# Performance work log

Measured on AMD Instinct MI355X. Metric: run time of the kernel, lower is better.

The kernel has to match this reference:

```python
import jax, jax.numpy as jnp
import numpy as np

N_NODES = 100000


def setup_inputs() -> dict:
    key = jax.random.key(0)
    ks = jax.random.split(key, 8)
    IN, HID, OUT = 128, 128, 64
    E = 1600000
    x = jax.random.normal(ks[0], (N_NODES, IN), dtype=jnp.float32)
    edge_index = jax.random.randint(ks[1], (2, E), 0, N_NODES, dtype=jnp.int64)
    # PyG SAGEConv params: lin_l (applied to aggregated neighbors, with bias),
    # lin_r (root weight, no bias).
    def lin(k, fi, fo):
        return jax.random.normal(k, (fi, fo), dtype=jnp.float32) / np.sqrt(fi)
    Wl0 = lin(ks[2], IN, HID)
    bl0 = jnp.zeros((HID,), dtype=jnp.float32)
    Wr0 = lin(ks[3], IN, HID)
    Wl1 = lin(ks[4], HID, OUT)
    bl1 = jnp.zeros((OUT,), dtype=jnp.float32)
    Wr1 = lin(ks[5], HID, OUT)
    return {"x": x, "edge_index": edge_index,
            "Wl0": Wl0, "bl0": bl0, "Wr0": Wr0,
            "Wl1": Wl1, "bl1": bl1, "Wr1": Wr1}


def _sage_conv(h, src, dst, Wl, bl, Wr):
    # mean aggregation of source features onto target nodes
    summed = jax.ops.segment_sum(h[src], dst, num_segments=N_NODES)  # [N, d]
    cnt = jax.ops.segment_sum(jnp.ones((src.shape[0], 1), h.dtype), dst,
                              num_segments=N_NODES)                  # [N, 1]
    agg = summed / jnp.maximum(cnt, 1.0)
    return agg @ Wl + bl + h @ Wr


def reference(x, edge_index, Wl0, bl0, Wr0, Wl1, bl1, Wr1):
    src, dst = edge_index[0], edge_index[1]
    h = jax.nn.relu(_sage_conv(x, src, dst, Wl0, bl0, Wr0))
    # dropout is identity in eval mode (training=False)
    return _sage_conv(h, src, dst, Wl1, bl1, Wr1)
```

## Files before the change

### kernel.cpp

```cpp
#include <hip/hip_runtime.h>


typedef short short8 __attribute__((ext_vector_type(8)));
typedef float f32x4 __attribute__((ext_vector_type(4)));
typedef float f32x2 __attribute__((ext_vector_type(2)));

#define NBUCK 782
#define BCAP  3072
#define EPB   8192

static __device__ __forceinline__ unsigned short f2bf(float f) {
    union { float f; unsigned u; } c; c.f = f;
    unsigned u = c.u + 0x7fffu + ((c.u >> 16) & 1u);
    return (unsigned short)(u >> 16);
}
static __device__ __forceinline__ float bf2f(unsigned short b) {
    union { unsigned u; float f; } c; c.u = ((unsigned)b) << 16;
    return c.f;
}
static __device__ __forceinline__ float bf2f_s(short b) {
    return bf2f((unsigned short)b);
}

static __device__ __forceinline__ unsigned char f2fp8(float x) {
    union { float f; unsigned u; } c; c.f = x;
    unsigned s = (c.u >> 24) & 0x80u;
    float a = __builtin_fabsf(x);
    if (a < 0.015625f) {
        int m = (int)rintf(a * 512.0f);
        return (unsigned char)(s | (unsigned)m);
    }
    unsigned u = c.u + 0x7ffffu + ((c.u >> 20) & 1u);
    int e = (int)((u >> 23) & 0xff) - 120;
    unsigned m = (u >> 20) & 7u;
    if (e > 15) { e = 15; m = 6; }
    return (unsigned char)(s | (unsigned)(e << 3) | m);
}

static __device__ __forceinline__ void acc_fp8x4(unsigned w, float* a) {
#if __has_builtin(__builtin_amdgcn_cvt_pk_f32_fp8)
    f32x2 lo = __builtin_amdgcn_cvt_pk_f32_fp8((int)w, false);
    f32x2 hi = __builtin_amdgcn_cvt_pk_f32_fp8((int)w, true);
    a[0] += lo[0]; a[1] += lo[1]; a[2] += hi[0]; a[3] += hi[1];
#else
    #pragma unroll
    for (int j = 0; j < 4; ++j) {
        unsigned b = (w >> (8 * j)) & 0xffu;
        union { unsigned u; float f; } c;
        c.u = ((b & 0x80u) << 24) | ((b & 0x7fu) << 20);
        a[j] += c.f * 0x1p120f;
    }
#endif
}

__global__ __launch_bounds__(256) void k_pack(const float* __restrict__ WA,
                                              const float* __restrict__ WB,
                                              int CA, int NC,
                                              unsigned short* __restrict__ Wp) {
    int tid = blockIdx.x * 256 + threadIdx.x;
    if (tid >= NC * 16) return;
    int lane = tid & 63, kk = (tid >> 6) & 3, tg = tid >> 8;
    int l15 = lane & 15, quad = lane >> 4;
    int c = tg * 16 + l15;
    const float* W = (c < CA) ? WA : WB;
    int cc = (c < CA) ? c : c - CA;
    short8 v;
    #pragma unroll
    for (int j = 0; j < 8; ++j) {
        int k = kk * 32 + quad * 8 + j;
        v[j] = (short)f2bf(W[(size_t)k * CA + cc]);
    }
    *(short8*)(Wp + (size_t)tid * 8) = v;
}

__global__ __launch_bounds__(256) void k_gemm0_bucket(
        const float* __restrict__ X, const unsigned short* __restrict__ Wp,
        unsigned char* __restrict__ P0, unsigned short* __restrict__ Q0, int Nrows,
        const int* __restrict__ src, const int* __restrict__ dst,
        int* __restrict__ cursor, int* __restrict__ bregion,
        int E, int gemmBlocks) {
    const int t = threadIdx.x;
    if ((int)blockIdx.x < gemmBlocks) {
        const int wave = t >> 6, lane = t & 63;
        const int quad = lane >> 4, l15 = lane & 15;
        const int row0 = blockIdx.x * 32;
        const int c0w = wave * 64;
        f32x4 acc[2][4];
        #pragma unroll
        for (int mt = 0; mt < 2; ++mt)
            #pragma unroll
            for (int tt = 0; tt < 4; ++tt) acc[mt][tt] = (f32x4){0.f, 0.f, 0.f, 0.f};
        #pragma unroll
        for (int kk = 0; kk < 4; ++kk) {
            const int k0 = kk * 32 + quad * 8;
            short8 a[2];
            #pragma unroll
            for (int mt = 0; mt < 2; ++mt) {
                int row = row0 + mt * 16 + l15;
                if (row > Nrows - 1) row = Nrows - 1;
                const float* xp = X + (size_t)row * 128 + k0;
                float4 f0 = *(const float4*)xp;
                float4 f1 = *(const float4*)(xp + 4);
                short8 v;
                v[0] = (short)f2bf(f0.x); v[1] = (short)f2bf(f0.y);
                v[2] = (short)f2bf(f0.z); v[3] = (short)f2bf(f0.w);
                v[4] = (short)f2bf(f1.x); v[5] = (short)f2bf(f1.y);
                v[6] = (short)f2bf(f1.z); v[7] = (short)f2bf(f1.w);
                a[mt] = v;
            }
            short8 b[4];
            #pragma unroll
            for (int tt = 0; tt < 4; ++tt) {
                int tg = (c0w >> 4) + tt;
                b[tt] = *(const short8*)(Wp + ((size_t)(tg * 4 + kk) * 64 + lane) * 8);
            }
            #pragma unroll
            for (int mt = 0; mt < 2; ++mt)
                #pragma unroll
                for (int tt = 0; tt < 4; ++tt)
                    acc[mt][tt] = __builtin_amdgcn_mfma_f32_16x16x32_bf16(
                        a[mt], b[tt], acc[mt][tt], 0, 0, 0);
        }
        #pragma unroll
        for (int mt = 0; mt < 2; ++mt)
            #pragma unroll
            for (int r = 0; r < 4; ++r) {
                int row = row0 + mt * 16 + quad * 4 + r;
                if (row < Nrows) {
                    if (c0w < 128) {
                        #pragma unroll
                        for (int tt = 0; tt < 4; ++tt)
                            P0[(size_t)row * 128 + c0w + tt * 16 + l15] =
                                f2fp8(acc[mt][tt][r]);
                    } else {
                        #pragma unroll
                        for (int tt = 0; tt < 4; ++tt)
                            Q0[(size_t)row * 128 + (c0w - 128) + tt * 16 + l15] =
                                f2bf(acc[mt][tt][r]);
                    }
                }
            }
        return;
    }
    __shared__ int hist[NBUCK];
    __shared__ int basel[NBUCK];
    int bid = blockIdx.x - gemmBlocks;
    for (int i = t; i < NBUCK; i += 256) hist[i] = 0;
    __syncthreads();
    int e0 = bid * EPB + t * 32;
    int d[32];
    if (e0 + 32 <= E) {
        #pragma unroll
        for (int q = 0; q < 8; ++q) {
            int4 v = *(const int4*)(dst + e0 + q * 4);
            d[q * 4 + 0] = v.x; d[q * 4 + 1] = v.y;
            d[q * 4 + 2] = v.z; d[q * 4 + 3] = v.w;
        }
    } else {
        #pragma unroll
        for (int j = 0; j < 32; ++j) d[j] = (e0 + j < E) ? dst[e0 + j] : -1;
    }
    #pragma unroll
    for (int j = 0; j < 32; ++j)
        if (d[j] >= 0) atomicAdd(&hist[d[j] >> 7], 1);
    __syncthreads();
    for (int i = t; i < NBUCK; i += 256) {
        int c = hist[i];
        basel[i] = (c > 0) ? atomicAdd(&cursor[i], c) : 0;
    }
    __syncthreads();
    for (int i = t; i < NBUCK; i += 256) hist[i] = 0;
    __syncthreads();
    int s[32];
    if (e0 + 32 <= E) {
        #pragma unroll
        for (int q = 0; q < 8; ++q) {
            int4 v = *(const int4*)(src + e0 + q * 4);
            s[q * 4 + 0] = v.x; s[q * 4 + 1] = v.y;
            s[q * 4 + 2] = v.z; s[q * 4 + 3] = v.w;
        }
    } else {
        #pragma unroll
        for (int j = 0; j < 32; ++j) s[j] = (e0 + j < E) ? src[e0 + j] : 0;
    }
    #pragma unroll
    for (int j = 0; j < 32; ++j) {
        if (d[j] < 0) continue;
        int b = d[j] >> 7;
        int r = atomicAdd(&hist[b], 1);
        bregion[(size_t)b * BCAP + basel[b] + r] = s[j] | ((d[j] & 127) << 20);
    }
}

__global__ __launch_bounds__(256) void k_csr(const int* __restrict__ cursor,
                                             const int* __restrict__ bregion,
                                             int* __restrict__ rowptr,
                                             int* __restrict__ csr, int Nn) {
    __shared__ int words[BCAP];
    __shared__ int hist[128], sc[128], rank[128];
    __shared__ int red[256];
    int b = blockIdx.x, t = threadIdx.x;
    int part = 0;
    for (int i = t; i < b; i += 256) part += cursor[i];
    red[t] = part;
    if (t < 128) { hist[t] = 0; rank[t] = 0; }
    __syncthreads();
    #pragma unroll
    for (int off = 128; off > 0; off >>= 1) {
        if (t < off) red[t] += red[t + off];
        __syncthreads();
    }
    int gbase = red[0];
    int cnt = cursor[b];
    for (int i = t; i < cnt; i += 256) {
        int w = bregion[(size_t)b * BCAP + i];
        words[i] = w;
        atomicAdd(&hist[w >> 20], 1);
    }
    __syncthreads();
    if (t < 128) sc[t] = hist[t];
    __syncthreads();
    #pragma unroll
    for (int off = 1; off < 128; off <<= 1) {
        int x = 0;
        if (t < 128 && t >= off) x = sc[t - off];
        __syncthreads();
        if (t < 128) sc[t] += x;
        __syncthreads();
    }
    if (t < 128) sc[t] -= hist[t];
    __syncthreads();
    if (t < 128) {
        int node = b * 128 + t;
        if (node <= Nn) rowptr[node] = gbase + sc[t];
    }
    for (int i = t; i < cnt; i += 256) {
        int w = words[i];
        int d7 = w >> 20;
        int r = atomicAdd(&rank[d7], 1);
        csr[gbase + sc[d7] + r] = w & 0xFFFFF;
    }
}

__global__ __launch_bounds__(256) void k_gemm1(const unsigned short* __restrict__ Xv,
                                               const unsigned short* __restrict__ Wp,
                                               unsigned char* __restrict__ P1,
                                               unsigned short* __restrict__ Q1,
                                               int Nrows) {
    const int t = threadIdx.x;
    const int wave = t >> 6, lane = t & 63;
    const int quad = lane >> 4, l15 = lane & 15;
    const int row0 = blockIdx.x * 32;
    const int c0w = wave * 32;
    f32x4 acc[2][2];
    #pragma unroll
    for (int mt = 0; mt < 2; ++mt)
        #pragma unroll
        for (int tt = 0; tt < 2; ++tt) acc[mt][tt] = (f32x4){0.f, 0.f, 0.f, 0.f};
    #pragma unroll
    for (int kk = 0; kk < 4; ++kk) {
        const int k0 = kk * 32 + quad * 8;
        short8 a[2];
        #pragma unroll
        for (int mt = 0; mt < 2; ++mt) {
            int row = row0 + mt * 16 + l15;
            if (row > Nrows - 1) row = Nrows - 1;
            a[mt] = *(const short8*)(Xv + (size_t)row * 128 + k0);
        }
        short8 b[2];
        #pragma unroll
        for (int tt = 0; tt < 2; ++tt) {
            int tg = (c0w >> 4) + tt;
            b[tt] = *(const short8*)(Wp + ((size_t)(tg * 4 + kk) * 64 + lane) * 8);
        }
        #pragma unroll
        for (int mt = 0; mt < 2; ++mt)
            #pragma unroll
            for (int tt = 0; tt < 2; ++tt)
                acc[mt][tt] = __builtin_amdgcn_mfma_f32_16x16x32_bf16(
                    a[mt], b[tt], acc[mt][tt], 0, 0, 0);
    }
    #pragma unroll
    for (int mt = 0; mt < 2; ++mt)
        #pragma unroll
        for (int r = 0; r < 4; ++r) {
            int row = row0 + mt * 16 + quad * 4 + r;
            if (row < Nrows) {
                if (c0w < 64) {
                    #pragma unroll
                    for (int tt = 0; tt < 2; ++tt)
                        P1[(size_t)row * 64 + c0w + tt * 16 + l15] =
                            f2fp8(acc[mt][tt][r]);
                } else {
                    #pragma unroll
                    for (int tt = 0; tt < 2; ++tt)
                        Q1[(size_t)row * 64 + (c0w - 64) + tt * 16 + l15] =
                            f2bf(acc[mt][tt][r]);
                }
            }
        }
}

__global__ __launch_bounds__(256) void k_agg0(const unsigned char* __restrict__ P0,
                                              const unsigned short* __restrict__ Q0,
                                              const int* __restrict__ rowptr,
                                              const int* __restrict__ csr,
                                              const float* __restrict__ bl0,
                                              unsigned short* __restrict__ h, int Nn) {
    int wave = threadIdx.x >> 6, lane = threadIdx.x & 63;
    int n = blockIdx.x * 4 + wave;
    if (n >= Nn) return;
    int g = lane >> 3, l7 = lane & 7;
    int st = rowptr[n], dg = rowptr[n + 1] - st;
    float acc[16] = {};
    int e = 0;
    for (; e + 16 <= dg; e += 16) {
        int s0 = csr[st + e + g];
        int s1 = csr[st + e + 8 + g];
        uint4 w0 = *(const uint4*)(P0 + (size_t)s0 * 128 + l7 * 16);
        uint4 w1 = *(const uint4*)(P0 + (size_t)s1 * 128 + l7 * 16);
        acc_fp8x4(w0.x, acc + 0);  acc_fp8x4(w0.y, acc + 4);
        acc_fp8x4(w0.z, acc + 8);  acc_fp8x4(w0.w, acc + 12);
        acc_fp8x4(w1.x, acc + 0);  acc_fp8x4(w1.y, acc + 4);
        acc_fp8x4(w1.z, acc + 8);  acc_fp8x4(w1.w, acc + 12);
    }
    for (; e + 8 <= dg; e += 8) {
        int s0 = csr[st + e + g];
        uint4 w0 = *(const uint4*)(P0 + (size_t)s0 * 128 + l7 * 16);
        acc_fp8x4(w0.x, acc + 0);  acc_fp8x4(w0.y, acc + 4);
        acc_fp8x4(w0.z, acc + 8);  acc_fp8x4(w0.w, acc + 12);
    }
    if (e + g < dg) {
        int s0 = csr[st + e + g];
        uint4 w0 = *(const uint4*)(P0 + (size_t)s0 * 128 + l7 * 16);
        acc_fp8x4(w0.x, acc + 0);  acc_fp8x4(w0.y, acc + 4);
        acc_fp8x4(w0.z, acc + 8);  acc_fp8x4(w0.w, acc + 12);
    }
    #pragma unroll
    for (int j = 0; j < 16; ++j) {
        acc[j] += __shfl_xor(acc[j], 8);
        acc[j] += __shfl_xor(acc[j], 16);
        acc[j] += __shfl_xor(acc[j], 32);
    }
    if (lane < 8) {
        float inv = 1.f / fmaxf((float)dg, 1.f);
        short8 q0 = *(const short8*)(Q0 + (size_t)n * 128 + l7 * 16);
        short8 q1 = *(const short8*)(Q0 + (size_t)n * 128 + l7 * 16 + 8);
        float bb[16];
        *(float4*)(bb + 0)  = *(const float4*)(bl0 + l7 * 16);
        *(float4*)(bb + 4)  = *(const float4*)(bl0 + l7 * 16 + 4);
        *(float4*)(bb + 8)  = *(const float4*)(bl0 + l7 * 16 + 8);
        *(float4*)(bb + 12) = *(const float4*)(bl0 + l7 * 16 + 12);
        short8 o0, o1;
        #pragma unroll
        for (int j = 0; j < 8; ++j) {
            float v = fmaxf(acc[j] * inv + bb[j] + bf2f_s(q0[j]), 0.f);
            o0[j] = (short)f2bf(v);
        }
        #pragma unroll
        for (int j = 0; j < 8; ++j) {
            float v = fmaxf(acc[8 + j] * inv + bb[8 + j] + bf2f_s(q1[j]), 0.f);
            o1[j] = (short)f2bf(v);
        }
        *(short8*)(h + (size_t)n * 128 + l7 * 16) = o0;
        *(short8*)(h + (size_t)n * 128 + l7 * 16 + 8) = o1;
    }
}

__global__ __launch_bounds__(256) void k_agg1(const unsigned char* __restrict__ P1,
                                              const unsigned short* __restrict__ Q1,
                                              const int* __restrict__ rowptr,
                                              const int* __restrict__ csr,
                                              const float* __restrict__ bl1,
                                              float* __restrict__ out, int Nn) {
    int wave = threadIdx.x >> 6, lane = threadIdx.x & 63;
    int n = blockIdx.x * 4 + wave;
    if (n >= Nn) return;
    int g = lane >> 2, l3 = lane & 3;
    int st = rowptr[n], dg = rowptr[n + 1] - st;
    float acc[16] = {};
    int e = 0;
    for (; e + 16 <= dg; e += 16) {
        int s0 = csr[st + e + g];
        uint4 w0 = *(const uint4*)(P1 + (size_t)s0 * 64 + l3 * 16);
        acc_fp8x4(w0.x, acc + 0);  acc_fp8x4(w0.y, acc + 4);
        acc_fp8x4(w0.z, acc + 8);  acc_fp8x4(w0.w, acc + 12);
    }
    if (e + g < dg) {
        int s0 = csr[st + e + g];
        uint4 w0 = *(const uint4*)(P1 + (size_t)s0 * 64 + l3 * 16);
        acc_fp8x4(w0.x, acc + 0);  acc_fp8x4(w0.y, acc + 4);
        acc_fp8x4(w0.z, acc + 8);  acc_fp8x4(w0.w, acc + 12);
    }
    #pragma unroll
    for (int j = 0; j < 16; ++j) {
        acc[j] += __shfl_xor(acc[j], 4);
        acc[j] += __shfl_xor(acc[j], 8);
        acc[j] += __shfl_xor(acc[j], 16);
        acc[j] += __shfl_xor(acc[j], 32);
    }
    if (lane < 4) {
        float inv = 1.f / fmaxf((float)dg, 1.f);
        short8 q0 = *(const short8*)(Q1 + (size_t)n * 64 + l3 * 16);
        short8 q1 = *(const short8*)(Q1 + (size_t)n * 64 + l3 * 16 + 8);
        float bb[16];
        *(float4*)(bb + 0)  = *(const float4*)(bl1 + l3 * 16);
        *(float4*)(bb + 4)  = *(const float4*)(bl1 + l3 * 16 + 4);
        *(float4*)(bb + 8)  = *(const float4*)(bl1 + l3 * 16 + 8);
        *(float4*)(bb + 12) = *(const float4*)(bl1 + l3 * 16 + 12);
        float4 o[4];
        #pragma unroll
        for (int j = 0; j < 8; ++j)
            ((float*)o)[j] = acc[j] * inv + bb[j] + bf2f_s(q0[j]);
        #pragma unroll
        for (int j = 0; j < 8; ++j)
            ((float*)o)[8 + j] = acc[8 + j] * inv + bb[8 + j] + bf2f_s(q1[j]);
        #pragma unroll
        for (int q = 0; q < 4; ++q)
            *(float4*)(out + (size_t)n * 64 + l3 * 16 + q * 4) = o[q];
    }
}

extern "C" void kernel_launch(void* const* d_in, const int* in_sizes, int n_in,
                              void* d_out, int out_size, void* d_ws, size_t ws_size,
                              hipStream_t stream) {
    const float* x   = (const float*)d_in[0];
    const int* eidx  = (const int*)d_in[1];
    const float* Wl0 = (const float*)d_in[2];
    const float* bl0 = (const float*)d_in[3];
    const float* Wr0 = (const float*)d_in[4];
    const float* Wl1 = (const float*)d_in[5];
    const float* bl1 = (const float*)d_in[6];
    const float* Wr1 = (const float*)d_in[7];
    float* out = (float*)d_out;

    const int N = in_sizes[0] / 128;
    const int E = in_sizes[1] / 2;
    const int* src = eidx;
    const int* dst = eidx + E;

    int* rowptr  = (int*)d_ws;
    int* cursor  = rowptr + (N + 4);
    int* bregion = cursor + 784;
    int* csr     = bregion + (size_t)NBUCK * BCAP;
    unsigned short* Wp0 = (unsigned short*)(csr + E);
    unsigned short* Wp1 = Wp0 + 32768;
    unsigned char*  P0  = (unsigned char*)(Wp1 + 16384);
    unsigned short* Q0  = (unsigned short*)(P0 + (size_t)N * 128);
    unsigned short* h   = Q0 + (size_t)N * 128;
    unsigned char*  P1  = (unsigned char*)(h + (size_t)N * 128);
    unsigned short* Q1  = (unsigned short*)(P1 + (size_t)N * 64);

    hipMemsetAsync(cursor, 0, NBUCK * sizeof(int), stream);

    k_pack<<<(256 * 16 + 255) / 256, 256, 0, stream>>>(Wl0, Wr0, 128, 256, Wp0);
    k_pack<<<(128 * 16 + 255) / 256, 256, 0, stream>>>(Wl1, Wr1, 64, 128, Wp1);

    int gemmBlocks = (N + 31) / 32;
    int nbb = (E + EPB - 1) / EPB;
    k_gemm0_bucket<<<gemmBlocks + nbb, 256, 0, stream>>>(
        x, Wp0, P0, Q0, N, src, dst, cursor, bregion, E, gemmBlocks);
    k_csr<<<NBUCK, 256, 0, stream>>>(cursor, bregion, rowptr, csr, N);

    k_agg0<<<(N + 3) / 4, 256, 0, stream>>>(P0, Q0, rowptr, csr, bl0, h, N);
    k_gemm1<<<(N + 31) / 32, 256, 0, stream>>>(h, Wp1, P1, Q1, N);
    k_agg1<<<(N + 3) / 4, 256, 0, stream>>>(P1, Q1, rowptr, csr, bl1, out, N);
}
```

Measured before the change: 327.7 us.

## Map one node per lane-group in aggregation kernels instead of one node per wave

Both aggregation kernels now assign each 8-lane (layer 0) or 4-lane (layer 1) group its own destination node, so a wave handles 8 or 16 nodes instead of one. Each group walks its own edge list serially, two edges at a time, and the cross-lane shuffle reduction over edges is removed. The goal is to stop wasting lanes when a node has fewer edges than lanes (average degree is about 16) and to drop the reduction cost. In exchange, lanes in a wave can diverge when node degrees differ, and the csr index loads are now scalar-dependent per group.

```diff
diff --git a/kernel.cpp b/kernel.cpp
--- a/kernel.cpp
+++ b/kernel.cpp
@@ -51,6 +51,10 @@
         a[j] += c.f * 0x1p120f;
     }
 #endif
+}
+static __device__ __forceinline__ void acc_row16(uint4 w, float* a) {
+    acc_fp8x4(w.x, a + 0);  acc_fp8x4(w.y, a + 4);
+    acc_fp8x4(w.z, a + 8);  acc_fp8x4(w.w, a + 12);
 }
 
 __global__ __launch_bounds__(256) void k_pack(const float* __restrict__ WA,
@@ -308,41 +312,27 @@
                                               const float* __restrict__ bl0,
                                               unsigned short* __restrict__ h, int Nn) {
     int wave = threadIdx.x >> 6, lane = threadIdx.x & 63;
-    int n = blockIdx.x * 4 + wave;
-    if (n >= Nn) return;
     int g = lane >> 3, l7 = lane & 7;
-    int st = rowptr[n], dg = rowptr[n + 1] - st;
+    int n = (blockIdx.x * 4 + wave) * 8 + g;
+    bool live = (n < Nn);
+    int st = 0, dg = 0;
+    if (live) { st = rowptr[n]; dg = rowptr[n + 1] - st; }
     float acc[16] = {};
     int e = 0;
-    for (; e + 16 <= dg; e += 16) {
-        int s0 = csr[st + e + g];
-        int s1 = csr[st + e + 8 + g];
+    for (; e + 2 <= dg; e += 2) {
+        int s0 = csr[st + e];
+        int s1 = csr[st + e + 1];
         uint4 w0 = *(const uint4*)(P0 + (size_t)s0 * 128 + l7 * 16);
         uint4 w1 = *(const uint4*)(P0 + (size_t)s1 * 128 + l7 * 16);
-        acc_fp8x4(w0.x, acc + 0);  acc_fp8x4(w0.y, acc + 4);
-        acc_fp8x4(w0.z, acc + 8);  acc_fp8x4(w0.w, acc + 12);
-        acc_fp8x4(w1.x, acc + 0);  acc_fp8x4(w1.y, acc + 4);
-        acc_fp8x4(w1.z, acc + 8);  acc_fp8x4(w1.w, acc + 12);
-    }
-    for (; e + 8 <= dg; e += 8) {
-        int s0 = csr[st + e + g];
+        acc_row16(w0, acc);
+        acc_row16(w1, acc);
+    }
+    if (e < dg) {
+        int s0 = csr[st + e];
         uint4 w0 = *(const uint4*)(P0 + (size_t)s0 * 128 + l7 * 16);
-        acc_fp8x4(w0.x, acc + 0);  acc_fp8x4(w0.y, acc + 4);
-        acc_fp8x4(w0.z, acc + 8);  acc_fp8x4(w0.w, acc + 12);
-    }
-    if (e + g < dg) {
-        int s0 = csr[st + e + g];
-        uint4 w0 = *(const uint4*)(P0 + (size_t)s0 * 128 + l7 * 16);
-        acc_fp8x4(w0.x, acc + 0);  acc_fp8x4(w0.y, acc + 4);
-        acc_fp8x4(w0.z, acc + 8);  acc_fp8x4(w0.w, acc + 12);
-    }
-    #pragma unroll
-    for (int j = 0; j < 16; ++j) {
-        acc[j] += __shfl_xor(acc[j], 8);
-        acc[j] += __shfl_xor(acc[j], 16);
-        acc[j] += __shfl_xor(acc[j], 32);
-    }
-    if (lane < 8) {
+        acc_row16(w0, acc);
+    }
+    if (live) {
         float inv = 1.f / fmaxf((float)dg, 1.f);
         short8 q0 = *(const short8*)(Q0 + (size_t)n * 128 + l7 * 16);
         short8 q1 = *(const short8*)(Q0 + (size_t)n * 128 + l7 * 16 + 8);
@@ -353,15 +343,11 @@
         *(float4*)(bb + 12) = *(const float4*)(bl0 + l7 * 16 + 12);
         short8 o0, o1;
         #pragma unroll
-        for (int j = 0; j < 8; ++j) {
-            float v = fmaxf(acc[j] * inv + bb[j] + bf2f_s(q0[j]), 0.f);
-            o0[j] = (short)f2bf(v);
-        }
-        #pragma unroll
-        for (int j = 0; j < 8; ++j) {
-            float v = fmaxf(acc[8 + j] * inv + bb[8 + j] + bf2f_s(q1[j]), 0.f);
-            o1[j] = (short)f2bf(v);
-        }
+        for (int j = 0; j < 8; ++j)
+            o0[j] = (short)f2bf(fmaxf(acc[j] * inv + bb[j] + bf2f_s(q0[j]), 0.f));
+        #pragma unroll
+        for (int j = 0; j < 8; ++j)
+            o1[j] = (short)f2bf(fmaxf(acc[8 + j] * inv + bb[8 + j] + bf2f_s(q1[j]), 0.f));
         *(short8*)(h + (size_t)n * 128 + l7 * 16) = o0;
         *(short8*)(h + (size_t)n * 128 + l7 * 16 + 8) = o1;
     }
@@ -374,32 +360,27 @@
                                               const float* __restrict__ bl1,
                                               float* __restrict__ out, int Nn) {
     int wave = threadIdx.x >> 6, lane = threadIdx.x & 63;
-    int n = blockIdx.x * 4 + wave;
-    if (n >= Nn) return;
     int g = lane >> 2, l3 = lane & 3;
-    int st = rowptr[n], dg = rowptr[n + 1] - st;
+    int n = (blockIdx.x * 4 + wave) * 16 + g;
+    bool live = (n < Nn);
+    int st = 0, dg = 0;
+    if (live) { st = rowptr[n]; dg = rowptr[n + 1] - st; }
     float acc[16] = {};
     int e = 0;
-    for (; e + 16 <= dg; e += 16) {
-        int s0 = csr[st + e + g];
+    for (; e + 2 <= dg; e += 2) {
+        int s0 = csr[st + e];
+        int s1 = csr[st + e + 1];
         uint4 w0 = *(const uint4*)(P1 + (size_t)s0 * 64 + l3 * 16);
-        acc_fp8x4(w0.x, acc + 0);  acc_fp8x4(w0.y, acc + 4);
-        acc_fp8x4(w0.z, acc + 8);  acc_fp8x4(w0.w, acc + 12);
-    }
-    if (e + g < dg) {
-        int s0 = csr[st + e + g];
+        uint4 w1 = *(const uint4*)(P1 + (size_t)s1 * 64 + l3 * 16);
+        acc_row16(w0, acc);
+        acc_row16(w1, acc);
+    }
+    if (e < dg) {
+        int s0 = csr[st + e];
         uint4 w0 = *(const uint4*)(P1 + (size_t)s0 * 64 + l3 * 16);
-        acc_fp8x4(w0.x, acc + 0);  acc_fp8x4(w0.y, acc + 4);
-        acc_fp8x4(w0.z, acc + 8);  acc_fp8x4(w0.w, acc + 12);
-    }
-    #pragma unroll
-    for (int j = 0; j < 16; ++j) {
-        acc[j] += __shfl_xor(acc[j], 4);
-        acc[j] += __shfl_xor(acc[j], 8);
-        acc[j] += __shfl_xor(acc[j], 16);
-        acc[j] += __shfl_xor(acc[j], 32);
-    }
-    if (lane < 4) {
+        acc_row16(w0, acc);
+    }
+    if (live) {
         float inv = 1.f / fmaxf((float)dg, 1.f);
         short8 q0 = *(const short8*)(Q1 + (size_t)n * 64 + l3 * 16);
         short8 q1 = *(const short8*)(Q1 + (size_t)n * 64 + l3 * 16 + 8);
@@ -462,7 +443,7 @@
         x, Wp0, P0, Q0, N, src, dst, cursor, bregion, E, gemmBlocks);
     k_csr<<<NBUCK, 256, 0, stream>>>(cursor, bregion, rowptr, csr, N);
 
-    k_agg0<<<(N + 3) / 4, 256, 0, stream>>>(P0, Q0, rowptr, csr, bl0, h, N);
+    k_agg0<<<(N + 31) / 32, 256, 0, stream>>>(P0, Q0, rowptr, csr, bl0, h, N);
     k_gemm1<<<(N + 31) / 32, 256, 0, stream>>>(h, Wp1, P1, Q1, N);
-    k_agg1<<<(N + 3) / 4, 256, 0, stream>>>(P1, Q1, rowptr, csr, bl1, out, N);
-}
+    k_agg1<<<(N + 63) / 64, 256, 0, stream>>>(P1, Q1, rowptr, csr, bl1, out, N);
+}
```

Measured after the change: 297.7 us. -9.1%, faster.
